# Performance work log

Hardware: AMD Instinct MI355X
Metric: run time of the kernel (lower is better)

Reference implementation:

```python
import jax, jax.numpy as jnp
import numpy as np

L, D, H, N, R = 4, 256, 512, 16, 8  # layers, d_model, hidden=2*d_model, state_dim, dt_rank
OUT_LEN, IN_DIM = 96, 32
EPS = 1e-5


def _layernorm(v, g, b):
    m = jnp.mean(v, axis=-1, keepdims=True)
    var = jnp.mean((v - m) ** 2, axis=-1, keepdims=True)
    return (v - m) / jnp.sqrt(var + EPS) * g + b


def _pos_encoding(T, d):
    pos = jnp.arange(T, dtype=jnp.float32)[:, None]
    div = jnp.exp(jnp.arange(0, d, 2, dtype=jnp.float32) * (-np.log(10000.0) / d))
    pe = jnp.zeros((T, d), dtype=jnp.float32)
    pe = pe.at[:, 0::2].set(jnp.sin(pos * div))
    pe = pe.at[:, 1::2].set(jnp.cos(pos * div))
    return pe


def setup_inputs() -> dict:
    key = jax.random.key(0)
    ks = jax.random.split(key, 20)
    inp = {
        "x": jax.random.normal(ks[0], (8, 1024, IN_DIM), dtype=jnp.float32),
        "emb_w": jax.random.normal(ks[1], (D, IN_DIM), dtype=jnp.float32) * 0.1,
        "emb_b": jnp.zeros((D,), dtype=jnp.float32),
        "norm_g": jnp.ones((L, D), dtype=jnp.float32),
        "norm_b": jnp.zeros((L, D), dtype=jnp.float32),
        "in_w": jax.random.normal(ks[2], (L, H, D), dtype=jnp.float32) * (1.0 / np.sqrt(D)),
        "conv_w": jax.random.normal(ks[3], (L, H, 1, 3), dtype=jnp.float32) * 0.5,
        "A_p": jax.random.normal(ks[4], (L, H, N), dtype=jnp.float32) * 0.01,
        "D_p": jnp.ones((L, H), dtype=jnp.float32),
        "dt1_w": jax.random.normal(ks[5], (L, R, H), dtype=jnp.float32) * (1.0 / np.sqrt(H)),
        "dt1_b": jnp.zeros((L, R), dtype=jnp.float32),
        "dt2_w": jax.random.normal(ks[6], (L, H, R), dtype=jnp.float32) * (1.0 / np.sqrt(R)),
        "dt2_b": jnp.zeros((L, H), dtype=jnp.float32),
        "out_w": jax.random.normal(ks[7], (L, D, H), dtype=jnp.float32) * (1.0 / np.sqrt(H)),
        "final_g": jnp.ones((D,), dtype=jnp.float32),
        "final_b": jnp.zeros((D,), dtype=jnp.float32),
        "head1_w": jax.random.normal(ks[8], (D, D), dtype=jnp.float32) * (1.0 / np.sqrt(D)),
        "head1_b": jnp.zeros((D,), dtype=jnp.float32),
        "head2_w": jax.random.normal(ks[9], (OUT_LEN, D), dtype=jnp.float32) * (1.0 / np.sqrt(D)),
        "head2_b": jnp.zeros((OUT_LEN,), dtype=jnp.float32),
    }
    return inp


def _mamba_block(h, g, b, in_w, conv_w, A_p, D_p, dt1_w, dt1_b, dt2_w, dt2_b, out_w):
    res = h
    v = _layernorm(h, g, b)            # [B,T,D]
    v = jnp.einsum('btd,hd->bth', v, in_w)  # [B,T,H]
    # depthwise conv1d, kernel 3, padding 1, groups=H
    vc = jnp.transpose(v, (0, 2, 1))   # [B,H,T]
    vc = jax.lax.conv_general_dilated(vc, conv_w, window_strides=(1,),
                                      padding=[(1, 1)], feature_group_count=H,
                                      dimension_numbers=('NCH', 'OIH', 'NCH'))
    v = jnp.transpose(jax.nn.silu(vc), (0, 2, 1))  # [B,T,H]
    dt = jax.nn.relu(jnp.einsum('bth,rh->btr', v, dt1_w) + dt1_b)
    dt = jnp.einsum('btr,hr->bth', dt, dt2_w) + dt2_b
    dt = jax.nn.softplus(dt)           # [B,T,H]
    A = -jnp.exp(A_p)                  # [H,N]
    safe_A = jnp.where(jnp.abs(A) < 1e-5, jnp.ones_like(A), A)

    B_sz = v.shape[0]
    state0 = jnp.zeros((B_sz, H, N), dtype=v.dtype)

    def step(state, inp):
        x_t, dt_t = inp  # [B,H] each
        dA = A * dt_t[..., None]            # [B,H,N]
        discA = jnp.exp(dA)
        discB = (discA - 1.0) / safe_A * dt_t[..., None]
        state = discA * state + discB * x_t[..., None]
        y = jnp.einsum('bhn,hn->bh', state, A_p) + D_p * x_t
        return state, y

    xs = (jnp.transpose(v, (1, 0, 2)), jnp.transpose(dt, (1, 0, 2)))  # [T,B,H]
    _, ys = jax.lax.scan(step, state0, xs)
    y = jnp.transpose(ys, (1, 0, 2))   # [B,T,H]
    return res + jnp.einsum('bth,dh->btd', y, out_w)


def reference(x, emb_w, emb_b, norm_g, norm_b, in_w, conv_w, A_p, D_p,
              dt1_w, dt1_b, dt2_w, dt2_b, out_w, final_g, final_b,
              head1_w, head1_b, head2_w, head2_b):
    h = jnp.einsum('bti,di->btd', x, emb_w) + emb_b  # [B,T,D]
    h = h + _pos_encoding(h.shape[1], D)[None]
    for l in range(L):
        h = _mamba_block(h, norm_g[l], norm_b[l], in_w[l], conv_w[l], A_p[l],
                         D_p[l], dt1_w[l], dt1_b[l], dt2_w[l], dt2_b[l], out_w[l])
    h = _layernorm(h, final_g, final_b)
    h = h[:, -1, :]                    # last token [B,D]
    h = jax.nn.silu(h @ head1_w.T + head1_b)
    return h @ head2_w.T + head2_b     # [B, OUT_LEN]
```

## Files before the change

kernel.cpp:

```cpp
#include <hip/hip_runtime.h>
#include <hip/hip_bf16.h>
#include <math.h>

#define BB 8
#define TT 1024
#define DD 256
#define HH 512
#define NN 16
#define RR 8
#define OUT_LEN 96
#define IN_DIM 32
#define MM (BB*TT)

#define SC 32
#define CC (TT/SC)

typedef unsigned short u16;
typedef unsigned int u32;
typedef __attribute__((ext_vector_type(8))) short short8;
typedef __attribute__((ext_vector_type(8))) unsigned short u16x8;
typedef __attribute__((ext_vector_type(4))) float float4v;

__device__ __forceinline__ u16 f2bf(float f) {
    __hip_bfloat16 h = __float2bfloat16(f);
    return *(u16*)&h;
}
__device__ __forceinline__ float bf2f(u16 u) {
    u32 v = ((u32)u) << 16;
    return *(float*)&v;
}

#define GLD_LDS16(src, dst) __builtin_amdgcn_global_load_lds( \
    (const __attribute__((address_space(1))) void*)(src),     \
    (__attribute__((address_space(3))) void*)(dst), 16, 0, 0)

__global__ __launch_bounds__(256) void embed_kernel(
    const float* __restrict__ x, const float* __restrict__ emb_w,
    const float* __restrict__ emb_b, float* __restrict__ h)
{
    int bt = blockIdx.x;
    int d  = threadIdx.x;
    int t  = bt & (TT - 1);

    __shared__ float xs[IN_DIM];
    if (threadIdx.x < IN_DIM) xs[threadIdx.x] = x[bt * IN_DIM + threadIdx.x];
    __syncthreads();

    const float* w = emb_w + d * IN_DIM;
    float acc = emb_b[d];
#pragma unroll
    for (int i = 0; i < IN_DIM; i++) acc = fmaf(xs[i], w[i], acc);

    int i2 = d & ~1;
    float div = expf(-(float)i2 * (logf(10000.0f) / (float)DD));
    float arg = (float)t * div;
    float pe = (d & 1) ? cosf(arg) : sinf(arg);
    h[bt * DD + d] = acc + pe;
}

__global__ __launch_bounds__(256) void cvt_bf16_kernel(
    const float* __restrict__ in, u16* __restrict__ out, int n)
{
    int i = blockIdx.x * 256 + threadIdx.x;
    if (i < n) out[i] = f2bf(in[i]);
}

__global__ __launch_bounds__(256) void ln_kernel(
    const float* __restrict__ h, const float* __restrict__ g,
    const float* __restrict__ b, u16* __restrict__ out)
{
    int bt = blockIdx.x;
    int d  = threadIdx.x;
    float v = h[bt * DD + d];

    __shared__ float red[4], red2[4];
    float s = v;
#pragma unroll
    for (int o = 32; o > 0; o >>= 1) s += __shfl_down(s, o);
    int lane = d & 63, wave = d >> 6;
    if (lane == 0) red[wave] = s;
    __syncthreads();
    float mean = (red[0] + red[1] + red[2] + red[3]) * (1.0f / DD);

    float c = v - mean;
    float s2 = c * c;
#pragma unroll
    for (int o = 32; o > 0; o >>= 1) s2 += __shfl_down(s2, o);
    if (lane == 0) red2[wave] = s2;
    __syncthreads();
    float var = (red2[0] + red2[1] + red2[2] + red2[3]) * (1.0f / DD);

    out[bt * DD + d] = f2bf(c * rsqrtf(var + 1e-5f) * g[d] + b[d]);
}

template<int BM, int BN, int OUT_BF16>
__global__ __launch_bounds__(256) void gemm_bf16(
    const u16* __restrict__ A, const u16* __restrict__ B,
    void* __restrict__ Cv, int M, int N, int K, int addC)
{
    constexpr int BK = 64;
    constexpr int MT = BM / 32;
    constexpr int NT = BN / 32;
    static_assert(BN == 64, "B staging assumes BN==64");

    __shared__ __align__(16) u16 Al[8][BM][8];
    __shared__ __align__(16) u16 Bl[8][BN][8];

    const int tid = threadIdx.x;
    const int bm = blockIdx.y * BM;
    const int bn = blockIdx.x * BN;
    const int wid = tid >> 6, lane = tid & 63;
    const int wm = wid >> 1, wn = wid & 1;
    const int lq = lane >> 4, lm = lane & 15;

    float4v acc[MT][NT];
#pragma unroll
    for (int i = 0; i < MT; i++)
#pragma unroll
        for (int j = 0; j < NT; j++) acc[i][j] = (float4v){0.f, 0.f, 0.f, 0.f};

    for (int k0 = 0; k0 < K; k0 += BK) {
#pragma unroll
        for (int it = 0; it < (8 * BM) / 256; it++) {
            int c = it * 256 + tid;
            int q = c / BM, row = c % BM;
            GLD_LDS16(A + (size_t)(bm + row) * K + k0 + q * 8, &Al[q][row][0]);
        }
#pragma unroll
        for (int it = 0; it < (8 * BN) / 256; it++) {
            int c = it * 256 + tid;
            int q = c / BN, row = c % BN;
            GLD_LDS16(B + (size_t)(bn + row) * K + k0 + q * 8, &Bl[q][row][0]);
        }
        __syncthreads();

        short8 af[2][MT], bf[2][NT];
#pragma unroll
        for (int kk = 0; kk < 2; kk++) {
#pragma unroll
            for (int mt = 0; mt < MT; mt++)
                af[kk][mt] = *(const short8*)&Al[kk * 4 + lq][wm * (BM / 2) + mt * 16 + lm][0];
#pragma unroll
            for (int nt = 0; nt < NT; nt++)
                bf[kk][nt] = *(const short8*)&Bl[kk * 4 + lq][wn * (BN / 2) + nt * 16 + lm][0];
        }

#pragma unroll
        for (int kk = 0; kk < 2; kk++)
#pragma unroll
            for (int mt = 0; mt < MT; mt++)
#pragma unroll
                for (int nt = 0; nt < NT; nt++)
                    acc[mt][nt] = __builtin_amdgcn_mfma_f32_16x16x32_bf16(
                        af[kk][mt], bf[kk][nt], acc[mt][nt], 0, 0, 0);
        __syncthreads();
    }

#pragma unroll
    for (int mt = 0; mt < MT; mt++)
#pragma unroll
        for (int nt = 0; nt < NT; nt++) {
            int row0 = bm + wm * (BM / 2) + mt * 16 + lq * 4;
            int col  = bn + wn * (BN / 2) + nt * 16 + lm;
#pragma unroll
            for (int r = 0; r < 4; r++) {
                float vv = acc[mt][nt][r];
                if (OUT_BF16) {
                    ((u16*)Cv)[(size_t)(row0 + r) * N + col] = f2bf(vv);
                } else {
                    float* cp = (float*)Cv + (size_t)(row0 + r) * N + col;
                    if (addC) vv += *cp;
                    *cp = vv;
                }
            }
        }
}

__global__ __launch_bounds__(256) void conv_silu_kernel(
    const u16* __restrict__ v, const float* __restrict__ w,
    u16* __restrict__ out)
{
    int base = (blockIdx.x * 256 + threadIdx.x) * 8;
    int h0 = base & (HH - 1);
    int t  = (base >> 9) & (TT - 1);

    u16x8 x0 = *(const u16x8*)(v + base);
    u16x8 xm = (t > 0)      ? *(const u16x8*)(v + base - HH) : (u16x8)(0);
    u16x8 xp = (t < TT - 1) ? *(const u16x8*)(v + base + HH) : (u16x8)(0);

    const float* wp = w + h0 * 3;
    u16x8 o;
#pragma unroll
    for (int j = 0; j < 8; j++) {
        float a = wp[j * 3] * bf2f(xm[j]);
        a = fmaf(wp[j * 3 + 1], bf2f(x0[j]), a);
        a = fmaf(wp[j * 3 + 2], bf2f(xp[j]), a);
        o[j] = f2bf(a / (1.0f + __expf(-a)));
    }
    *(u16x8*)(out + base) = o;
}

__global__ __launch_bounds__(256) void dt1_kernel(
    const u16* __restrict__ vs, const float* __restrict__ w,
    const float* __restrict__ bias, float* __restrict__ dtr)
{
    int wave = threadIdx.x >> 6;
    int lane = threadIdx.x & 63;
    int m = blockIdx.x * 4 + wave;
    const u16* vrow = vs + (size_t)m * HH;

    float acc[RR];
#pragma unroll
    for (int r = 0; r < RR; r++) acc[r] = 0.0f;

#pragma unroll
    for (int j = 0; j < HH / 64; j++) {
        int hh = j * 64 + lane;
        float vv = bf2f(vrow[hh]);
#pragma unroll
        for (int r = 0; r < RR; r++) acc[r] = fmaf(vv, w[r * HH + hh], acc[r]);
    }
#pragma unroll
    for (int r = 0; r < RR; r++) {
#pragma unroll
        for (int o = 32; o > 0; o >>= 1) acc[r] += __shfl_down(acc[r], o);
    }
    if (lane == 0) {
#pragma unroll
        for (int r = 0; r < RR; r++)
            dtr[m * RR + r] = fmaxf(acc[r] + bias[r], 0.0f);
    }
}

__device__ __forceinline__ float softplus_f(float s) {
    return (s > 20.0f) ? s : __logf(1.0f + __expf(s));
}

__global__ __launch_bounds__(256) void scan_pass1(
    const u16* __restrict__ vs,
    const float* __restrict__ dtr,
    const float* __restrict__ dt2_w,
    const float* __restrict__ dt2_b,
    const float* __restrict__ A_p,
    float* __restrict__ Lst,
    float* __restrict__ sdt)
{
    int h = blockIdx.x * 256 + threadIdx.x;
    int c = blockIdx.y;
    int b = blockIdx.z;

    float A[NN], invA[NN], st[NN];
    const float* ap = A_p + h * NN;
#pragma unroll
    for (int n = 0; n < NN; n++) {
        float a = -__expf(ap[n]);
        A[n] = a; invA[n] = 1.0f / a; st[n] = 0.0f;
    }
    float w2[RR];
#pragma unroll
    for (int r = 0; r < RR; r++) w2[r] = dt2_w[h * RR + r];
    float b2 = dt2_b[h];

    const u16*   vbase = vs  + ((size_t)b * TT + (size_t)c * SC) * HH + h;
    const float* drow  = dtr + ((size_t)b * TT + (size_t)c * SC) * RR;

    float dr[RR];
#pragma unroll
    for (int r = 0; r < RR; r++) dr[r] = drow[r];

    float s_dt = 0.0f;
#pragma unroll 2
    for (int t = 0; t < SC; t++) {
        float drn[RR];
        if (t + 1 < SC) {
#pragma unroll
            for (int r = 0; r < RR; r++) drn[r] = drow[(t + 1) * RR + r];
        }
        float s = b2;
#pragma unroll
        for (int r = 0; r < RR; r++) s = fmaf(dr[r], w2[r], s);
        float dt = softplus_f(s);
        float xv = bf2f(vbase[(size_t)t * HH]);
        s_dt += dt;
#pragma unroll
        for (int n = 0; n < NN; n++) {
            float e  = __expf(A[n] * dt);
            float dB = (e - 1.0f) * invA[n] * dt;
            st[n] = fmaf(e, st[n], dB * xv);
        }
#pragma unroll
        for (int r = 0; r < RR; r++) dr[r] = drn[r];
    }

    size_t base = (((size_t)c * BB + b) * HH + h) * NN;
#pragma unroll
    for (int n = 0; n < NN; n += 4)
        *(float4*)(Lst + base + n) = make_float4(st[n], st[n+1], st[n+2], st[n+3]);
    sdt[((size_t)c * BB + b) * HH + h] = s_dt;
}

__global__ __launch_bounds__(256) void scan_carry(
    const float* __restrict__ A_p, const float* __restrict__ sdt,
    float* __restrict__ Lst)
{
    int i = blockIdx.x * 256 + threadIdx.x;
    int n  = i & (NN - 1);
    int bh = i >> 4;
    int h  = bh & (HH - 1);
    int b  = bh >> 9;

    float A = -__expf(A_p[h * NN + n]);
    float E = 0.0f;
#pragma unroll
    for (int c = 0; c < CC; c++) {
        size_t sidx = ((size_t)c * BB + b) * HH + h;
        float P = __expf(A * sdt[sidx]);
        size_t lidx = sidx * NN + n;
        float Lc = Lst[lidx];
        Lst[lidx] = E;
        E = fmaf(P, E, Lc);
    }
}

__global__ __launch_bounds__(256) void scan_pass2(
    const u16* __restrict__ vs,
    const float* __restrict__ dtr,
    const float* __restrict__ dt2_w,
    const float* __restrict__ dt2_b,
    const float* __restrict__ A_p, const float* __restrict__ D_p,
    const float* __restrict__ carry,
    u16* __restrict__ y)
{
    int h = blockIdx.x * 256 + threadIdx.x;
    int c = blockIdx.y;
    int b = blockIdx.z;

    float A[NN], invA[NN], Ap[NN], st[NN];
    const float* app = A_p + h * NN;
    size_t cbase = (((size_t)c * BB + b) * HH + h) * NN;
#pragma unroll
    for (int n = 0; n < NN; n += 4) {
        float4 c4 = *(const float4*)(carry + cbase + n);
        st[n] = c4.x; st[n+1] = c4.y; st[n+2] = c4.z; st[n+3] = c4.w;
    }
#pragma unroll
    for (int n = 0; n < NN; n++) {
        float apv = app[n];
        Ap[n] = apv;
        float a = -__expf(apv);
        A[n] = a; invA[n] = 1.0f / a;
    }
    float w2[RR];
#pragma unroll
    for (int r = 0; r < RR; r++) w2[r] = dt2_w[h * RR + r];
    float b2 = dt2_b[h];
    float Dp = D_p[h];

    const u16*   vbase = vs  + ((size_t)b * TT + (size_t)c * SC) * HH + h;
    const float* drow  = dtr + ((size_t)b * TT + (size_t)c * SC) * RR;
    u16*         ybase = y   + ((size_t)b * TT + (size_t)c * SC) * HH + h;

    float dr[RR];
#pragma unroll
    for (int r = 0; r < RR; r++) dr[r] = drow[r];

#pragma unroll 2
    for (int t = 0; t < SC; t++) {
        float drn[RR];
        if (t + 1 < SC) {
#pragma unroll
            for (int r = 0; r < RR; r++) drn[r] = drow[(t + 1) * RR + r];
        }
        float s = b2;
#pragma unroll
        for (int r = 0; r < RR; r++) s = fmaf(dr[r], w2[r], s);
        float dt = softplus_f(s);
        float xv = bf2f(vbase[(size_t)t * HH]);
        float acc = Dp * xv;
#pragma unroll
        for (int n = 0; n < NN; n++) {
            float e  = __expf(A[n] * dt);
            float dB = (e - 1.0f) * invA[n] * dt;
            st[n] = fmaf(e, st[n], dB * xv);
            acc = fmaf(st[n], Ap[n], acc);
        }
        ybase[(size_t)t * HH] = f2bf(acc);
#pragma unroll
        for (int r = 0; r < RR; r++) dr[r] = drn[r];
    }
}

__global__ __launch_bounds__(256) void head_kernel(
    const float* __restrict__ h,
    const float* __restrict__ fg, const float* __restrict__ fb,
    const float* __restrict__ w1, const float* __restrict__ b1,
    const float* __restrict__ w2, const float* __restrict__ b2,
    float* __restrict__ out)
{
    int b = blockIdx.x;
    int d = threadIdx.x;
    __shared__ float hn[DD], s1[DD];
    __shared__ float red[4];

    float v = h[((size_t)b * TT + (TT - 1)) * DD + d];

    float s = v;
#pragma unroll
    for (int o = 32; o > 0; o >>= 1) s += __shfl_down(s, o);
    int lane = d & 63, wave = d >> 6;
    if (lane == 0) red[wave] = s;
    __syncthreads();
    float mean = (red[0] + red[1] + red[2] + red[3]) * (1.0f / DD);
    __syncthreads();

    float c = v - mean;
    float s2 = c * c;
#pragma unroll
    for (int o = 32; o > 0; o >>= 1) s2 += __shfl_down(s2, o);
    if (lane == 0) red[wave] = s2;
    __syncthreads();
    float var = (red[0] + red[1] + red[2] + red[3]) * (1.0f / DD);

    hn[d] = c * rsqrtf(var + 1e-5f) * fg[d] + fb[d];
    __syncthreads();

    float a1 = b1[d];
    const float* w1r = w1 + d * DD;
#pragma unroll 8
    for (int k = 0; k < DD; k++) a1 = fmaf(hn[k], w1r[k], a1);
    s1[d] = a1 / (1.0f + __expf(-a1));
    __syncthreads();

    if (d < OUT_LEN) {
        float a2 = b2[d];
        const float* w2r = w2 + d * DD;
#pragma unroll 8
        for (int k = 0; k < DD; k++) a2 = fmaf(s1[k], w2r[k], a2);
        out[b * OUT_LEN + d] = a2;
    }
}

extern "C" void kernel_launch(void* const* d_in, const int* in_sizes, int n_in,
                              void* d_out, int out_size, void* d_ws, size_t ws_size,
                              hipStream_t stream)
{
    (void)in_sizes; (void)n_in; (void)out_size; (void)ws_size;

    const float* x       = (const float*)d_in[0];
    const float* emb_w   = (const float*)d_in[1];
    const float* emb_b   = (const float*)d_in[2];
    const float* norm_g  = (const float*)d_in[3];
    const float* norm_b  = (const float*)d_in[4];
    const float* in_w    = (const float*)d_in[5];
    const float* conv_w  = (const float*)d_in[6];
    const float* A_p     = (const float*)d_in[7];
    const float* D_p     = (const float*)d_in[8];
    const float* dt1_w   = (const float*)d_in[9];
    const float* dt1_b   = (const float*)d_in[10];
    const float* dt2_w   = (const float*)d_in[11];
    const float* dt2_b   = (const float*)d_in[12];
    const float* out_w   = (const float*)d_in[13];
    const float* final_g = (const float*)d_in[14];
    const float* final_b = (const float*)d_in[15];
    const float* head1_w = (const float*)d_in[16];
    const float* head1_b = (const float*)d_in[17];
    const float* head2_w = (const float*)d_in[18];
    const float* head2_b = (const float*)d_in[19];
    float* outp = (float*)d_out;

    char* ws = (char*)d_ws;
    float* h    = (float*)ws;                 ws += (size_t)MM * DD * 4;
    u16*   vbf  = (u16*)ws;                   ws += (size_t)MM * HH * 2;
    u16*   vsb  = (u16*)ws;                   ws += (size_t)MM * HH * 2;
    u16*   yb_u = (u16*)ws;                   ws += (size_t)MM * HH * 2;
    float* dtr  = (float*)ws;                 ws += (size_t)MM * RR * 4;
    float* Lst  = (float*)ws;                 ws += (size_t)CC * BB * HH * NN * 4;
    float* sdt  = (float*)ws;                 ws += (size_t)CC * BB * HH * 4;
    u16*   wbf_in  = (u16*)ws;                ws += (size_t)4 * HH * DD * 2;
    u16*   wbf_out = (u16*)ws;                ws += (size_t)4 * DD * HH * 2;

    cvt_bf16_kernel<<<(4 * HH * DD) / 256, 256, 0, stream>>>(in_w,  wbf_in,  4 * HH * DD);
    cvt_bf16_kernel<<<(4 * DD * HH) / 256, 256, 0, stream>>>(out_w, wbf_out, 4 * DD * HH);

    embed_kernel<<<MM, 256, 0, stream>>>(x, emb_w, emb_b, h);

    for (int l = 0; l < 4; l++) {
        ln_kernel<<<MM, 256, 0, stream>>>(h, norm_g + l * DD, norm_b + l * DD, yb_u);
        gemm_bf16<128, 64, 1><<<dim3(HH / 64, MM / 128), 256, 0, stream>>>(
            yb_u, wbf_in + (size_t)l * HH * DD, vbf, MM, HH, DD, 0);
        conv_silu_kernel<<<(MM * HH) / (256 * 8), 256, 0, stream>>>(
            vbf, conv_w + (size_t)l * HH * 3, vsb);
        dt1_kernel<<<MM / 4, 256, 0, stream>>>(
            vsb, dt1_w + (size_t)l * RR * HH, dt1_b + l * RR, dtr);

        scan_pass1<<<dim3(HH / 256, CC, BB), 256, 0, stream>>>(
            vsb, dtr, dt2_w + (size_t)l * HH * RR, dt2_b + l * HH,
            A_p + (size_t)l * HH * NN, Lst, sdt);
        scan_carry<<<(BB * HH * NN) / 256, 256, 0, stream>>>(
            A_p + (size_t)l * HH * NN, sdt, Lst);
        scan_pass2<<<dim3(HH / 256, CC, BB), 256, 0, stream>>>(
            vsb, dtr, dt2_w + (size_t)l * HH * RR, dt2_b + l * HH,
            A_p + (size_t)l * HH * NN, D_p + l * HH, Lst, yb_u);

        gemm_bf16<64, 64, 0><<<dim3(DD / 64, MM / 64), 256, 0, stream>>>(
            yb_u, wbf_out + (size_t)l * DD * HH, h, MM, DD, HH, 1);
    }

    head_kernel<<<BB, 256, 0, stream>>>(h, final_g, final_b,
                                        head1_w, head1_b, head2_w, head2_b, outp);
}
```

Measured before the change: 540.4 us.

## Fuse conv+dt1 and embed+LN, merge weight casts, shrink scan chunk

Merges conv_silu and the dt1 projection into one kernel that computes the SiLU-convolved row in registers and reduces the rank-8 projection straight from them, with dt1 weights staged in LDS. This removes a full re-read of vsb per layer. The embedding kernel now also emits the first layer's LayerNorm, the two weight-cast kernels become one launch, and the scan chunk length drops from 32 to 16 so there are more parallel chunks. The shorter chunk doubles the carry loop length and the Lst/sdt traffic, and the carry loop is no longer unrolled.

After: 535.8 us. About the same (-0.8%).

```diff
diff --git a/kernel.cpp b/kernel.cpp
--- a/kernel.cpp
+++ b/kernel.cpp
@@ -12,7 +12,7 @@
 #define IN_DIM 32
 #define MM (BB*TT)
 
-#define SC 32
+#define SC 16
 #define CC (TT/SC)
 
 typedef unsigned short u16;
@@ -34,15 +34,18 @@
     (const __attribute__((address_space(1))) void*)(src),     \
     (__attribute__((address_space(3))) void*)(dst), 16, 0, 0)
 
-__global__ __launch_bounds__(256) void embed_kernel(
+__global__ __launch_bounds__(256) void embed_ln_kernel(
     const float* __restrict__ x, const float* __restrict__ emb_w,
-    const float* __restrict__ emb_b, float* __restrict__ h)
+    const float* __restrict__ emb_b,
+    const float* __restrict__ g, const float* __restrict__ b,
+    float* __restrict__ h, u16* __restrict__ lnout)
 {
     int bt = blockIdx.x;
     int d  = threadIdx.x;
     int t  = bt & (TT - 1);
 
     __shared__ float xs[IN_DIM];
+    __shared__ float red[4], red2[4];
     if (threadIdx.x < IN_DIM) xs[threadIdx.x] = x[bt * IN_DIM + threadIdx.x];
     __syncthreads();
 
@@ -55,14 +58,35 @@
     float div = expf(-(float)i2 * (logf(10000.0f) / (float)DD));
     float arg = (float)t * div;
     float pe = (d & 1) ? cosf(arg) : sinf(arg);
-    h[bt * DD + d] = acc + pe;
+    float val = acc + pe;
+    h[bt * DD + d] = val;
+
+    float s = val;
+#pragma unroll
+    for (int o = 32; o > 0; o >>= 1) s += __shfl_down(s, o);
+    int lane = d & 63, wave = d >> 6;
+    if (lane == 0) red[wave] = s;
+    __syncthreads();
+    float mean = (red[0] + red[1] + red[2] + red[3]) * (1.0f / DD);
+
+    float c = val - mean;
+    float s2 = c * c;
+#pragma unroll
+    for (int o = 32; o > 0; o >>= 1) s2 += __shfl_down(s2, o);
+    if (lane == 0) red2[wave] = s2;
+    __syncthreads();
+    float var = (red2[0] + red2[1] + red2[2] + red2[3]) * (1.0f / DD);
+
+    lnout[bt * DD + d] = f2bf(c * rsqrtf(var + 1e-5f) * g[d] + b[d]);
 }
 
 __global__ __launch_bounds__(256) void cvt_bf16_kernel(
-    const float* __restrict__ in, u16* __restrict__ out, int n)
+    const float* __restrict__ in1, u16* __restrict__ out1, int n1,
+    const float* __restrict__ in2, u16* __restrict__ out2, int n2)
 {
     int i = blockIdx.x * 256 + threadIdx.x;
-    if (i < n) out[i] = f2bf(in[i]);
+    if (i < n1) out1[i] = f2bf(in1[i]);
+    else if (i < n1 + n2) out2[i - n1] = f2bf(in2[i - n1]);
 }
 
 __global__ __launch_bounds__(256) void ln_kernel(
@@ -176,59 +200,77 @@
         }
 }
 
-__global__ __launch_bounds__(256) void conv_silu_kernel(
-    const u16* __restrict__ v, const float* __restrict__ w,
-    u16* __restrict__ out)
-{
-    int base = (blockIdx.x * 256 + threadIdx.x) * 8;
-    int h0 = base & (HH - 1);
-    int t  = (base >> 9) & (TT - 1);
-
-    u16x8 x0 = *(const u16x8*)(v + base);
-    u16x8 xm = (t > 0)      ? *(const u16x8*)(v + base - HH) : (u16x8)(0);
-    u16x8 xp = (t < TT - 1) ? *(const u16x8*)(v + base + HH) : (u16x8)(0);
-
-    const float* wp = w + h0 * 3;
+__global__ __launch_bounds__(256) void conv_dt1_kernel(
+    const u16* __restrict__ v,
+    const float* __restrict__ cwg,
+    const float* __restrict__ w1g,
+    const float* __restrict__ b1g,
+    u16* __restrict__ vsb,
+    float* __restrict__ dtr)
+{
+    __shared__ float w1s[RR * 2 * 256];
+    int tid = threadIdx.x;
+    {
+        int lane = tid & 63, rc = tid >> 6;
+#pragma unroll
+        for (int i = 0; i < 4; i++) {
+            int rci = rc + i * 4;
+            int r = rci >> 1, jc = rci & 1;
+            float4 wv = *(const float4*)(w1g + r * HH + lane * 8 + jc * 4);
+            *(float4*)&w1s[rci * 256 + lane * 4] = wv;
+        }
+    }
+    __syncthreads();
+
+    int wave = tid >> 6, lane = tid & 63;
+    int m = blockIdx.x * 4 + wave;
+    int t = m & (TT - 1);
+    int h0 = lane * 8;
+
+    const u16* vrow = v + (size_t)m * HH + h0;
+    u16x8 x0 = *(const u16x8*)vrow;
+    u16x8 xm = (t > 0)      ? *(const u16x8*)(vrow - HH) : (u16x8)(0);
+    u16x8 xp = (t < TT - 1) ? *(const u16x8*)(vrow + HH) : (u16x8)(0);
+
+    const float* wp = cwg + h0 * 3;
+    float a[8];
     u16x8 o;
 #pragma unroll
     for (int j = 0; j < 8; j++) {
-        float a = wp[j * 3] * bf2f(xm[j]);
-        a = fmaf(wp[j * 3 + 1], bf2f(x0[j]), a);
-        a = fmaf(wp[j * 3 + 2], bf2f(xp[j]), a);
-        o[j] = f2bf(a / (1.0f + __expf(-a)));
-    }
-    *(u16x8*)(out + base) = o;
-}
-
-__global__ __launch_bounds__(256) void dt1_kernel(
-    const u16* __restrict__ vs, const float* __restrict__ w,
-    const float* __restrict__ bias, float* __restrict__ dtr)
-{
-    int wave = threadIdx.x >> 6;
-    int lane = threadIdx.x & 63;
-    int m = blockIdx.x * 4 + wave;
-    const u16* vrow = vs + (size_t)m * HH;
+        float s = wp[j * 3] * bf2f(xm[j]);
+        s = fmaf(wp[j * 3 + 1], bf2f(x0[j]), s);
+        s = fmaf(wp[j * 3 + 2], bf2f(xp[j]), s);
+        s = s / (1.0f + __expf(-s));
+        a[j] = s;
+        o[j] = f2bf(s);
+    }
+    *(u16x8*)(vsb + (size_t)m * HH + h0) = o;
 
     float acc[RR];
 #pragma unroll
-    for (int r = 0; r < RR; r++) acc[r] = 0.0f;
-
-#pragma unroll
-    for (int j = 0; j < HH / 64; j++) {
-        int hh = j * 64 + lane;
-        float vv = bf2f(vrow[hh]);
-#pragma unroll
-        for (int r = 0; r < RR; r++) acc[r] = fmaf(vv, w[r * HH + hh], acc[r]);
-    }
-#pragma unroll
     for (int r = 0; r < RR; r++) {
-#pragma unroll
-        for (int o = 32; o > 0; o >>= 1) acc[r] += __shfl_down(acc[r], o);
+        float4 wlo = *(const float4*)&w1s[(r * 2 + 0) * 256 + lane * 4];
+        float4 whi = *(const float4*)&w1s[(r * 2 + 1) * 256 + lane * 4];
+        float s = a[0] * wlo.x;
+        s = fmaf(a[1], wlo.y, s);
+        s = fmaf(a[2], wlo.z, s);
+        s = fmaf(a[3], wlo.w, s);
+        s = fmaf(a[4], whi.x, s);
+        s = fmaf(a[5], whi.y, s);
+        s = fmaf(a[6], whi.z, s);
+        s = fmaf(a[7], whi.w, s);
+        acc[r] = s;
+    }
+#pragma unroll
+    for (int r = 0; r < RR; r++) {
+#pragma unroll
+        for (int o2 = 1; o2 < 64; o2 <<= 1) acc[r] += __shfl_xor(acc[r], o2);
     }
     if (lane == 0) {
 #pragma unroll
-        for (int r = 0; r < RR; r++)
-            dtr[m * RR + r] = fmaxf(acc[r] + bias[r], 0.0f);
+        for (int r = 0; r < RR; r++) acc[r] = fmaxf(acc[r] + b1g[r], 0.0f);
+        *(float4*)(dtr + (size_t)m * RR)     = make_float4(acc[0], acc[1], acc[2], acc[3]);
+        *(float4*)(dtr + (size_t)m * RR + 4) = make_float4(acc[4], acc[5], acc[6], acc[7]);
     }
 }
 
@@ -311,7 +353,6 @@
 
     float A = -__expf(A_p[h * NN + n]);
     float E = 0.0f;
-#pragma unroll
     for (int c = 0; c < CC; c++) {
         size_t sidx = ((size_t)c * BB + b) * HH + h;
         float P = __expf(A * sdt[sidx]);
@@ -479,19 +520,19 @@
     u16*   wbf_in  = (u16*)ws;                ws += (size_t)4 * HH * DD * 2;
     u16*   wbf_out = (u16*)ws;                ws += (size_t)4 * DD * HH * 2;
 
-    cvt_bf16_kernel<<<(4 * HH * DD) / 256, 256, 0, stream>>>(in_w,  wbf_in,  4 * HH * DD);
-    cvt_bf16_kernel<<<(4 * DD * HH) / 256, 256, 0, stream>>>(out_w, wbf_out, 4 * DD * HH);
-
-    embed_kernel<<<MM, 256, 0, stream>>>(x, emb_w, emb_b, h);
+    const int NW = 4 * HH * DD;
+    cvt_bf16_kernel<<<(2 * NW) / 256, 256, 0, stream>>>(in_w, wbf_in, NW, out_w, wbf_out, NW);
+
+    embed_ln_kernel<<<MM, 256, 0, stream>>>(x, emb_w, emb_b, norm_g, norm_b, h, yb_u);
 
     for (int l = 0; l < 4; l++) {
-        ln_kernel<<<MM, 256, 0, stream>>>(h, norm_g + l * DD, norm_b + l * DD, yb_u);
+        if (l > 0)
+            ln_kernel<<<MM, 256, 0, stream>>>(h, norm_g + l * DD, norm_b + l * DD, yb_u);
         gemm_bf16<128, 64, 1><<<dim3(HH / 64, MM / 128), 256, 0, stream>>>(
             yb_u, wbf_in + (size_t)l * HH * DD, vbf, MM, HH, DD, 0);
-        conv_silu_kernel<<<(MM * HH) / (256 * 8), 256, 0, stream>>>(
-            vbf, conv_w + (size_t)l * HH * 3, vsb);
-        dt1_kernel<<<MM / 4, 256, 0, stream>>>(
-            vsb, dt1_w + (size_t)l * RR * HH, dt1_b + l * RR, dtr);
+        conv_dt1_kernel<<<MM / 4, 256, 0, stream>>>(
+            vbf, conv_w + (size_t)l * HH * 3,
+            dt1_w + (size_t)l * RR * HH, dt1_b + l * RR, vsb, dtr);
 
         scan_pass1<<<dim3(HH / 256, CC, BB), 256, 0, stream>>>(
             vsb, dtr, dt2_w + (size_t)l * HH * RR, dt2_b + l * HH,
```
